# Kernel optimization log

Hardware: AMD Instinct MI355X
Metric: run time of the kernel (lower is better)

## Reference

```python
import jax, jax.numpy as jnp
import numpy as np

OUT = 56          # roi_align / mask resolution
SCALE = 0.25      # spatial_scale (bases at stride 4)
CO = 14           # raw coefficient resolution


def _roi_align_one(feat, box):
    """torchvision roi_align, aligned=True, sampling_ratio=1.
    feat: [B, H, W] base maps for this roi's image; box: [4] = (x0,y0,x1,y1).
    Returns [B, OUT, OUT]."""
    H, W = feat.shape[1], feat.shape[2]
    s = box * SCALE - 0.5  # aligned=True half-pixel offset
    x0, y0, x1, y1 = s[0], s[1], s[2], s[3]
    bw = (x1 - x0) / OUT
    bh = (y1 - y0) / OUT
    # sampling_ratio=1 -> single sample at each bin center
    xs = x0 + (jnp.arange(OUT, dtype=feat.dtype) + 0.5) * bw
    ys = y0 + (jnp.arange(OUT, dtype=feat.dtype) + 0.5) * bh
    vy = (ys >= -1.0) & (ys <= H)
    vx = (xs >= -1.0) & (xs <= W)
    yc = jnp.clip(ys, 0.0, H - 1)
    xc = jnp.clip(xs, 0.0, W - 1)
    yl = jnp.clip(jnp.floor(yc).astype(jnp.int32), 0, H - 2); yh = yl + 1
    xl = jnp.clip(jnp.floor(xc).astype(jnp.int32), 0, W - 2); xh = xl + 1
    ly = yc - yl; hy = 1.0 - ly
    lx = xc - xl; hx = 1.0 - lx
    fll = feat[:, yl, :][:, :, xl]; flh = feat[:, yl, :][:, :, xh]
    fhl = feat[:, yh, :][:, :, xl]; fhh = feat[:, yh, :][:, :, xh]
    val = (hy[:, None] * (hx[None, :] * fll + lx[None, :] * flh)
           + ly[:, None] * (hx[None, :] * fhl + lx[None, :] * fhh))
    return val * (vy[:, None] & vx[None, :])


def _paste_masks(masks, boxes, img_h, img_w):
    """do_paste_mask: grid_sample(bilinear, align_corners=False, zero pad).
    The grid is separable (y depends on row, x on column), so express it as two
    batched matmuls with tent-kernel weights. masks: [N,56,56] -> [N,img_h,img_w]."""
    x0, y0, x1, y1 = (boxes[:, 0:1], boxes[:, 1:2], boxes[:, 2:3], boxes[:, 3:4])
    gy = ((jnp.arange(img_h, dtype=masks.dtype) + 0.5 - y0) / (y1 - y0)) * 2.0 - 1.0  # [N,H]
    gx = ((jnp.arange(img_w, dtype=masks.dtype) + 0.5 - x0) / (x1 - x0)) * 2.0 - 1.0  # [N,W]
    # unnormalize (align_corners=False): f = (g+1)*size/2 - 0.5
    fy = (gy + 1.0) * OUT * 0.5 - 0.5
    fx = (gx + 1.0) * OUT * 0.5 - 0.5
    idx = jnp.arange(OUT, dtype=masks.dtype)
    Wy = jnp.maximum(0.0, 1.0 - jnp.abs(fy[:, :, None] - idx))  # [N, img_h, 56]
    Wx = jnp.maximum(0.0, 1.0 - jnp.abs(fx[:, :, None] - idx))  # [N, img_w, 56]
    rows = jnp.einsum('nhm,nmw->nhw', Wy, masks)                # [N, img_h, 56]
    return jnp.einsum('nhw,nqw->nhq', rows, Wx)                 # [N, img_h, img_w]


def setup_inputs() -> dict:
    key = jax.random.key(0)
    ks = jax.random.split(key, 6)
    b_h, b_w = 136, 200                 # bases at stride 4 of a 544x800 image
    img_h, img_w = b_h * 4, b_w * 4
    N, Bb = 100, 4
    bases = jax.random.normal(ks[0], (1, Bb, b_h, b_w), jnp.float32)
    x0 = jax.random.uniform(ks[1], (N, 1), minval=0.0, maxval=img_w * 0.55)
    y0 = jax.random.uniform(ks[2], (N, 1), minval=0.0, maxval=img_h * 0.55)
    w = jax.random.uniform(ks[3], (N, 1), minval=32.0, maxval=img_w * 0.4)
    h = jax.random.uniform(ks[4], (N, 1), minval=32.0, maxval=img_h * 0.4)
    boxes = jnp.concatenate([x0, y0,
                             jnp.minimum(x0 + w, img_w - 1.0),
                             jnp.minimum(y0 + h, img_h - 1.0)], axis=1)
    top = jax.random.normal(ks[5], (N, Bb * CO * CO), jnp.float32)
    box_feat = jnp.concatenate([jnp.zeros((N, 1), jnp.float32), boxes, top], axis=1)
    return {"bases": bases, "box_feat": box_feat}


def reference(bases, box_feat):
    bidx = box_feat[:, 0].astype(jnp.int32)
    boxes = box_feat[:, 1:5]
    top_feat = box_feat[:, 5:]
    N = box_feat.shape[0]
    Bb, b_h, b_w = bases.shape[1], bases.shape[2], bases.shape[3]
    # roi_align over all detections
    rois = jax.vmap(lambda i, b: _roi_align_one(bases[i], b))(bidx, boxes)  # [N,B,56,56]
    # merge_bases: upsample 14->56 (bilinear, align_corners=False), softmax over bases, blend
    coeffs = top_feat.reshape(N, Bb, CO, CO)
    coeffs = jax.image.resize(coeffs, (N, Bb, OUT, OUT), method='bilinear')
    coeffs = jax.nn.softmax(coeffs, axis=1)
    masks = jax.nn.sigmoid(jnp.sum(rois * coeffs, axis=1))  # [N,56,56]
    return _paste_masks(masks, boxes, b_h * 4, b_w * 4)      # [N, 4*b_h, 4*b_w]
```

## Files before the change

### kernel.cpp

```cpp
#include <hip/hip_runtime.h>
#include <math.h>

#define OUTD 56
#define COD  14
#define BH   136
#define BW   200
#define IMGH 544
#define IMGW 800
#define BB   4
#define BFS  789

__global__ __launch_bounds__(256) void mask_kernel(
    const float* __restrict__ bases,
    const float* __restrict__ box_feat,
    float* __restrict__ masks) {
  const int n = blockIdx.y;
  const int p = blockIdx.x * 256 + threadIdx.x;
  if (p >= OUTD * OUTD) return;
  const int y = p / OUTD;
  const int x = p - y * OUTD;

  const float* bf = box_feat + (size_t)n * BFS;
  const int bidx = (int)bf[0];
  const float x0 = bf[1], y0 = bf[2], x1 = bf[3], y1 = bf[4];
  const float sx0 = x0 * 0.25f - 0.5f;
  const float sy0 = y0 * 0.25f - 0.5f;
  const float bwv = (x1 - x0) * 0.25f * (1.0f / OUTD);
  const float bhv = (y1 - y0) * 0.25f * (1.0f / OUTD);
  const float* feat = bases + (size_t)bidx * BB * BH * BW;
  const float* top  = bf + 5;

  const float ysv = sy0 + ((float)y + 0.5f) * bhv;
  const float xsv = sx0 + ((float)x + 0.5f) * bwv;
  const float valid =
      (ysv >= -1.0f && ysv <= (float)BH && xsv >= -1.0f && xsv <= (float)BW)
          ? 1.0f : 0.0f;
  const float yc = fminf(fmaxf(ysv, 0.0f), (float)(BH - 1));
  const float xc = fminf(fmaxf(xsv, 0.0f), (float)(BW - 1));
  int yl = (int)floorf(yc); yl = yl > (BH - 2) ? (BH - 2) : yl;
  int xl = (int)floorf(xc); xl = xl > (BW - 2) ? (BW - 2) : xl;
  const float ly = yc - (float)yl, hy = 1.0f - ly;
  const float lx = xc - (float)xl, hx = 1.0f - lx;
  const float w00 = hy * hx, w01 = hy * lx, w10 = ly * hx, w11 = ly * lx;

  float cyf = fminf(fmaxf(((float)y + 0.5f) * 0.25f - 0.5f, 0.0f), (float)(COD - 1));
  float cxf = fminf(fmaxf(((float)x + 0.5f) * 0.25f - 0.5f, 0.0f), (float)(COD - 1));
  int cyl = (int)floorf(cyf); cyl = cyl > (COD - 2) ? (COD - 2) : cyl;
  int cxl = (int)floorf(cxf); cxl = cxl > (COD - 2) ? (COD - 2) : cxl;
  const float cly = cyf - (float)cyl, chy = 1.0f - cly;
  const float clx = cxf - (float)cxl, chx = 1.0f - clx;
  const float cw00 = chy * chx, cw01 = chy * clx, cw10 = cly * chx, cw11 = cly * clx;

  float rvals[BB], cvals[BB];
#pragma unroll
  for (int b = 0; b < BB; ++b) {
    const float* fb = feat + b * BH * BW;
    const float r = w00 * fb[yl * BW + xl]       + w01 * fb[yl * BW + xl + 1] +
                    w10 * fb[(yl + 1) * BW + xl] + w11 * fb[(yl + 1) * BW + xl + 1];
    rvals[b] = r * valid;
    const float* tb = top + b * COD * COD;
    cvals[b] = cw00 * tb[cyl * COD + cxl]       + cw01 * tb[cyl * COD + cxl + 1] +
               cw10 * tb[(cyl + 1) * COD + cxl] + cw11 * tb[(cyl + 1) * COD + cxl + 1];
  }

  const float mx = fmaxf(fmaxf(cvals[0], cvals[1]), fmaxf(cvals[2], cvals[3]));
  float e[BB], s = 0.0f;
#pragma unroll
  for (int b = 0; b < BB; ++b) { e[b] = __expf(cvals[b] - mx); s += e[b]; }
  const float inv = 1.0f / s;
  float dot = 0.0f;
#pragma unroll
  for (int b = 0; b < BB; ++b) dot += rvals[b] * (e[b] * inv);
  masks[(size_t)n * (OUTD * OUTD) + p] = 1.0f / (1.0f + __expf(-dot));
}

__global__ __launch_bounds__(256) void paste_kernel(
    const float* __restrict__ masks,
    const float* __restrict__ box_feat,
    float4* __restrict__ out) {
  const int h = blockIdx.x;
  const int n = blockIdx.y;
  const int tid = threadIdx.x;

  const float* bf = box_feat + (size_t)n * BFS;
  const float y0 = bf[2], y1 = bf[4];
  float4* orow = out + ((size_t)n * IMGH + h) * (IMGW / 4);

  const float fy = ((float)h + 0.5f - y0) * ((float)OUTD / (y1 - y0)) - 0.5f;

  if (!(fy > -1.0f && fy < (float)OUTD)) {
    if (tid < IMGW / 4) orow[tid] = make_float4(0.f, 0.f, 0.f, 0.f);
    return;
  }

  const int ml = (int)floorf(fy);
  const float wy1 = fy - (float)ml;
  const float wy0 = 1.0f - wy1;

  __shared__ float mrow[2][OUTD];
  if (tid < 2 * OUTD) {
    const int r_idx = (tid >= OUTD) ? 1 : 0;
    const int x = tid - r_idx * OUTD;
    const int r = ml + r_idx;
    float v = 0.0f;
    if (r >= 0 && r < OUTD)
      v = masks[(size_t)n * (OUTD * OUTD) + r * OUTD + x];
    mrow[r_idx][x] = v;
  }
  __syncthreads();

  if (tid >= IMGW / 4) return;

  const float x0 = bf[1], x1 = bf[3];
  const float invw = (float)OUTD / (x1 - x0);
  const float cx = (0.5f - x0) * invw - 0.5f;

  float res[4];
#pragma unroll
  for (int i = 0; i < 4; ++i) {
    const float q = (float)(tid * 4 + i);
    const float fx = fmaf(q, invw, cx);
    float v = 0.0f;
    if (fx > -1.0f && fx < (float)OUTD) {
      const int xl = (int)floorf(fx);
      float wx1 = fx - (float)xl;
      float wx0 = 1.0f - wx1;
      const int xls = xl < 0 ? 0 : xl;
      const int xhs = (xl + 1 > OUTD - 1) ? (OUTD - 1) : (xl + 1);
      if (xl < 0) wx0 = 0.0f;
      if (xl + 1 > OUTD - 1) wx1 = 0.0f;
      v = wy0 * (wx0 * mrow[0][xls] + wx1 * mrow[0][xhs]) +
          wy1 * (wx0 * mrow[1][xls] + wx1 * mrow[1][xhs]);
    }
    res[i] = v;
  }
  orow[tid] = make_float4(res[0], res[1], res[2], res[3]);
}

extern "C" void kernel_launch(void* const* d_in, const int* in_sizes, int n_in,
                              void* d_out, int out_size, void* d_ws, size_t ws_size,
                              hipStream_t stream) {
  const float* bases    = (const float*)d_in[0];
  const float* box_feat = (const float*)d_in[1];
  const int N = in_sizes[1] / BFS;

  float* masks = (float*)d_ws;

  dim3 g1((OUTD * OUTD + 255) / 256, N);
  mask_kernel<<<g1, 256, 0, stream>>>(bases, box_feat, masks);

  dim3 g2(IMGH, N);
  paste_kernel<<<g2, 256, 0, stream>>>(masks, box_feat, (float4*)d_out);
}
```

Before: 175.0 us.

## Zero output with memset and paste only the box-covered region

The whole output is now cleared with hipMemsetAsync, and the paste kernel launches a fixed MAXROWS blocks per detection starting just above the box, writing only the columns near the box's x-range. This is meant to avoid computing every pixel of the full 544x800 image per mask and to let a fast fill engine handle the zeros. In exchange, the interior writes become scalar rather than float4, and correctness depends on boxes never spanning more than MAXROWS rows (box height is capped at about 0.4 of the image height).

```diff
diff --git a/kernel.cpp b/kernel.cpp
--- a/kernel.cpp
+++ b/kernel.cpp
@@ -74,24 +74,24 @@
   masks[(size_t)n * (OUTD * OUTD) + p] = 1.0f / (1.0f + __expf(-dot));
 }
 
-__global__ __launch_bounds__(256) void paste_kernel(
+#define MAXROWS 226
+
+__global__ __launch_bounds__(256) void paste_interior(
     const float* __restrict__ masks,
     const float* __restrict__ box_feat,
-    float4* __restrict__ out) {
-  const int h = blockIdx.x;
+    float* __restrict__ out) {
   const int n = blockIdx.y;
   const int tid = threadIdx.x;
 
   const float* bf = box_feat + (size_t)n * BFS;
-  const float y0 = bf[2], y1 = bf[4];
-  float4* orow = out + ((size_t)n * IMGH + h) * (IMGW / 4);
+  const float x0 = bf[1], y0 = bf[2], x1 = bf[3], y1 = bf[4];
+
+  const int hs = max(0, (int)floorf(y0) - 3);
+  const int h  = hs + (int)blockIdx.x;
+  if (h >= IMGH) return;
 
   const float fy = ((float)h + 0.5f - y0) * ((float)OUTD / (y1 - y0)) - 0.5f;
-
-  if (!(fy > -1.0f && fy < (float)OUTD)) {
-    if (tid < IMGW / 4) orow[tid] = make_float4(0.f, 0.f, 0.f, 0.f);
-    return;
-  }
+  if (!(fy > -1.0f && fy < (float)OUTD)) return;
 
   const int ml = (int)floorf(fy);
   const float wy1 = fy - (float)ml;
@@ -109,17 +109,15 @@
   }
   __syncthreads();
 
-  if (tid >= IMGW / 4) return;
+  const int qs = max(0, (int)floorf(x0) - 4);
+  const int qe = min(IMGW - 1, (int)ceilf(x1) + 3);
 
-  const float x0 = bf[1], x1 = bf[3];
   const float invw = (float)OUTD / (x1 - x0);
-  const float cx = (0.5f - x0) * invw - 0.5f;
+  const float cxc = (0.5f - x0) * invw - 0.5f;
 
-  float res[4];
-#pragma unroll
-  for (int i = 0; i < 4; ++i) {
-    const float q = (float)(tid * 4 + i);
-    const float fx = fmaf(q, invw, cx);
+  float* orow = out + ((size_t)n * IMGH + h) * IMGW;
+  for (int q = qs + tid; q <= qe; q += 256) {
+    const float fx = fmaf((float)q, invw, cxc);
     float v = 0.0f;
     if (fx > -1.0f && fx < (float)OUTD) {
       const int xl = (int)floorf(fx);
@@ -132,9 +130,8 @@
       v = wy0 * (wx0 * mrow[0][xls] + wx1 * mrow[0][xhs]) +
           wy1 * (wx0 * mrow[1][xls] + wx1 * mrow[1][xhs]);
     }
-    res[i] = v;
+    orow[q] = v;
   }
-  orow[tid] = make_float4(res[0], res[1], res[2], res[3]);
 }
 
 extern "C" void kernel_launch(void* const* d_in, const int* in_sizes, int n_in,
@@ -146,9 +143,11 @@
 
   float* masks = (float*)d_ws;
 
+  hipMemsetAsync(d_out, 0, (size_t)out_size * sizeof(float), stream);
+
   dim3 g1((OUTD * OUTD + 255) / 256, N);
   mask_kernel<<<g1, 256, 0, stream>>>(bases, box_feat, masks);
 
-  dim3 g2(IMGH, N);
-  paste_kernel<<<g2, 256, 0, stream>>>(masks, box_feat, (float4*)d_out);
+  dim3 g2(MAXROWS, N);
+  paste_interior<<<g2, 256, 0, stream>>>(masks, box_feat, (float*)d_out);
 }
```

Result: slower. 183.0 us (+4.5%).

## Process eight output rows per block in paste kernel with full-mask shared staging

Applied to the files above, without the earlier changes.

The paste kernel now gives each block a group of eight image rows instead of one. All 256 threads stride over the 8x200 float4 elements, so the 56 threads per block that used to sit idle now do work. The whole 56x56 mask is staged in shared memory, replacing the two-row staging, and groups that fall entirely outside the box are zero-filled directly. This cuts the block count and per-block overhead and improves lane utilisation. In exchange, every non-empty block loads the full 12.5KB mask even when it needs only a few rows.

```diff
diff --git a/kernel.cpp b/kernel.cpp
--- a/kernel.cpp
+++ b/kernel.cpp
@@ -9,6 +9,9 @@
 #define IMGW 800
 #define BB   4
 #define BFS  789
+#define GRP  8
+#define W4   (IMGW / 4)
+#define ELEMS (GRP * W4)
 
 __global__ __launch_bounds__(256) void mask_kernel(
     const float* __restrict__ bases,
@@ -74,67 +77,81 @@
   masks[(size_t)n * (OUTD * OUTD) + p] = 1.0f / (1.0f + __expf(-dot));
 }
 
-__global__ __launch_bounds__(256) void paste_kernel(
+__global__ __launch_bounds__(256) void paste_group(
     const float* __restrict__ masks,
     const float* __restrict__ box_feat,
     float4* __restrict__ out) {
-  const int h = blockIdx.x;
-  const int n = blockIdx.y;
+  const int n  = blockIdx.y;
+  const int hs = (int)blockIdx.x * GRP;
   const int tid = threadIdx.x;
 
   const float* bf = box_feat + (size_t)n * BFS;
-  const float y0 = bf[2], y1 = bf[4];
-  float4* orow = out + ((size_t)n * IMGH + h) * (IMGW / 4);
+  const float x0 = bf[1], y0 = bf[2], x1 = bf[3], y1 = bf[4];
 
-  const float fy = ((float)h + 0.5f - y0) * ((float)OUTD / (y1 - y0)) - 0.5f;
+  float4* obase = out + ((size_t)n * IMGH + hs) * W4;
 
-  if (!(fy > -1.0f && fy < (float)OUTD)) {
-    if (tid < IMGW / 4) orow[tid] = make_float4(0.f, 0.f, 0.f, 0.f);
+  const float sy = (float)OUTD / (y1 - y0);
+  const float cyc_ = (0.5f - y0) * sy - 0.5f;
+  const float fy_first = (float)hs * sy + cyc_;
+  const float fy_last  = (float)(hs + GRP - 1) * sy + cyc_;
+
+  if (!(fy_last > -1.0f && fy_first < (float)OUTD)) {
+    const float4 z = make_float4(0.f, 0.f, 0.f, 0.f);
+    for (int idx = tid; idx < ELEMS; idx += 256) obase[idx] = z;
     return;
   }
 
-  const int ml = (int)floorf(fy);
-  const float wy1 = fy - (float)ml;
-  const float wy0 = 1.0f - wy1;
-
-  __shared__ float mrow[2][OUTD];
-  if (tid < 2 * OUTD) {
-    const int r_idx = (tid >= OUTD) ? 1 : 0;
-    const int x = tid - r_idx * OUTD;
-    const int r = ml + r_idx;
-    float v = 0.0f;
-    if (r >= 0 && r < OUTD)
-      v = masks[(size_t)n * (OUTD * OUTD) + r * OUTD + x];
-    mrow[r_idx][x] = v;
+  __shared__ float m[OUTD * OUTD];
+  {
+    const float* msrc = masks + (size_t)n * (OUTD * OUTD);
+    for (int i = tid; i < OUTD * OUTD; i += 256) m[i] = msrc[i];
   }
   __syncthreads();
 
-  if (tid >= IMGW / 4) return;
+  const float invw = (float)OUTD / (x1 - x0);
+  const float cxc = (0.5f - x0) * invw - 0.5f;
 
-  const float x0 = bf[1], x1 = bf[3];
-  const float invw = (float)OUTD / (x1 - x0);
-  const float cx = (0.5f - x0) * invw - 0.5f;
-
-  float res[4];
+  int row = tid / W4;
+  int col = tid - row * W4;
+  for (int idx = tid; idx < ELEMS; idx += 256) {
+    const float fy = (float)(hs + row) * sy + cyc_;
+    float4 o = make_float4(0.f, 0.f, 0.f, 0.f);
+    if (fy > -1.0f && fy < (float)OUTD) {
+      const int ml = (int)floorf(fy);
+      float wy1 = fy - (float)ml;
+      float wy0 = 1.0f - wy1;
+      const int r0 = ml < 0 ? 0 : ml;
+      const int r1 = (ml + 1 > OUTD - 1) ? (OUTD - 1) : (ml + 1);
+      if (ml < 0) wy0 = 0.0f;
+      if (ml + 1 > OUTD - 1) wy1 = 0.0f;
+      const float* row0 = &m[r0 * OUTD];
+      const float* row1 = &m[r1 * OUTD];
+      float res[4];
 #pragma unroll
-  for (int i = 0; i < 4; ++i) {
-    const float q = (float)(tid * 4 + i);
-    const float fx = fmaf(q, invw, cx);
-    float v = 0.0f;
-    if (fx > -1.0f && fx < (float)OUTD) {
-      const int xl = (int)floorf(fx);
-      float wx1 = fx - (float)xl;
-      float wx0 = 1.0f - wx1;
-      const int xls = xl < 0 ? 0 : xl;
-      const int xhs = (xl + 1 > OUTD - 1) ? (OUTD - 1) : (xl + 1);
-      if (xl < 0) wx0 = 0.0f;
-      if (xl + 1 > OUTD - 1) wx1 = 0.0f;
-      v = wy0 * (wx0 * mrow[0][xls] + wx1 * mrow[0][xhs]) +
-          wy1 * (wx0 * mrow[1][xls] + wx1 * mrow[1][xhs]);
+      for (int i = 0; i < 4; ++i) {
+        const float q = (float)(col * 4 + i);
+        const float fx = fmaf(q, invw, cxc);
+        float v = 0.0f;
+        if (fx > -1.0f && fx < (float)OUTD) {
+          const int xl = (int)floorf(fx);
+          float wx1 = fx - (float)xl;
+          float wx0 = 1.0f - wx1;
+          const int xls = xl < 0 ? 0 : xl;
+          const int xhs = (xl + 1 > OUTD - 1) ? (OUTD - 1) : (xl + 1);
+          if (xl < 0) wx0 = 0.0f;
+          if (xl + 1 > OUTD - 1) wx1 = 0.0f;
+          v = wy0 * (wx0 * row0[xls] + wx1 * row0[xhs]) +
+              wy1 * (wx0 * row1[xls] + wx1 * row1[xhs]);
+        }
+        res[i] = v;
+      }
+      o = make_float4(res[0], res[1], res[2], res[3]);
     }
-    res[i] = v;
+    obase[row * W4 + col] = o;
+    row += 1;
+    col += 56;
+    if (col >= W4) { col -= W4; row += 1; }
   }
-  orow[tid] = make_float4(res[0], res[1], res[2], res[3]);
 }
 
 extern "C" void kernel_launch(void* const* d_in, const int* in_sizes, int n_in,
@@ -149,6 +166,6 @@
   dim3 g1((OUTD * OUTD + 255) / 256, N);
   mask_kernel<<<g1, 256, 0, stream>>>(bases, box_feat, masks);
 
-  dim3 g2(IMGH, N);
-  paste_kernel<<<g2, 256, 0, stream>>>(masks, box_feat, (float4*)d_out);
+  dim3 g2(IMGH / GRP, N);
+  paste_group<<<g2, 256, 0, stream>>>(masks, box_feat, (float4*)d_out);
 }
```

New measurement: 180.0 us. 2.9% more time.
